# Kernel optimization log

Hardware: AMD Instinct MI355X
Metric: run time of the kernel (lower is better)

Reference implementation:

```python
import jax, jax.numpy as jnp
import numpy as np

N, C_S, C_Z, H, D = 512, 384, 128, 16, 24  # c_hidden per head
EPS = 1e-5

def _ln(x, g, b):
    m = jnp.mean(x, axis=-1, keepdims=True)
    v = jnp.mean(jnp.square(x - m), axis=-1, keepdims=True)
    return (x - m) * jax.lax.rsqrt(v + EPS) * g + b

def setup_inputs() -> dict:
    key = jax.random.key(0)
    ks = jax.random.split(key, 12)
    s = lambda fan: 1.0 / np.sqrt(fan)
    return {
        "a": jax.random.normal(ks[0], (1, N, C_S), jnp.float32),
        "z": jax.random.normal(ks[1], (1, N, N, C_Z), jnp.float32),
        "g_a": jnp.ones((C_S,), jnp.float32),
        "b_a": jnp.zeros((C_S,), jnp.float32),
        "g_z": jnp.ones((C_Z,), jnp.float32),
        "b_z": jnp.zeros((C_Z,), jnp.float32),
        "Wz": jax.random.normal(ks[2], (C_Z, H), jnp.float32) * s(C_Z),
        "bz": jnp.zeros((H,), jnp.float32),
        "Wq": jax.random.normal(ks[3], (C_S, H * D), jnp.float32) * s(C_S),
        "Wk": jax.random.normal(ks[4], (C_S, H * D), jnp.float32) * s(C_S),
        "Wv": jax.random.normal(ks[5], (C_S, H * D), jnp.float32) * s(C_S),
        "Wg": jax.random.normal(ks[6], (C_S, H * D), jnp.float32) * s(C_S),
        "bg": jnp.zeros((H * D,), jnp.float32),
        "Wo": jax.random.normal(ks[7], (H * D, C_S), jnp.float32) * s(H * D),
        "bo": jnp.zeros((C_S,), jnp.float32),
    }

def reference(a, z, g_a, b_a, g_z, b_z, Wz, bz, Wq, Wk, Wv, Wg, bg, Wo, bo):
    B = a.shape[0]
    a_n = _ln(a, g_a, b_a)                       # [B,N,C_S]
    z_n = _ln(z, g_z, b_z)                       # [B,N,N,C_Z]
    # linear_z then permute(0,3,1,2): [B,N,N,H] -> [B,H,N,N]
    pair_bias = jnp.einsum('bijc,ch->bhij', z_n, Wz) + bz[None, :, None, None]
    q = (a_n @ Wq).reshape(B, N, H, D) * (1.0 / np.sqrt(D))
    k = (a_n @ Wk).reshape(B, N, H, D)
    v = (a_n @ Wv).reshape(B, N, H, D)
    scores = jnp.einsum('bqhd,bkhd->bhqk', q, k) + pair_bias
    p = jax.nn.softmax(scores, axis=-1)
    o = jnp.einsum('bhqk,bkhd->bqhd', p, v)      # [B,N,H,D]
    g = jax.nn.sigmoid(a_n @ Wg + bg).reshape(B, N, H, D)
    o = (o * g).reshape(B, N, H * D)
    return o @ Wo + bo                            # [B,N,C_S]
```

## Files before the change

kernel.cpp:

```cpp
#include <hip/hip_runtime.h>
#include <math.h>

#define N 512
#define CS 384
#define CZ 128
#define NH 16
#define DH 24
#define HD 384
#define NN (N*N)
#define EPS 1e-5f

#define OFF_AN   0
#define OFF_QT   196608
#define OFF_KT   393216
#define OFF_VT   589824
#define OFF_GT   786432
#define OFF_OG   983040
#define OFF_WZ2  1179648
#define OFF_SH   1181696
#define OFF_BH   1181712
#define OFF_BIAS 1181728

__global__ void prep_kernel(const float* __restrict__ g_z, const float* __restrict__ lnb_z,
                            const float* __restrict__ Wz, const float* __restrict__ bz,
                            float* __restrict__ wz2, float* __restrict__ sh, float* __restrict__ bh) {
    int t = threadIdx.x;
    for (int i = t; i < NH * CZ; i += 256) {
        int h = i >> 7, c = i & (CZ - 1);
        wz2[h * CZ + c] = g_z[c] * Wz[c * NH + h];
    }
    __shared__ float ls[NH][17], lb[NH][17];
    int h = t >> 4, seg = t & 15;
    float s = 0.f, b = 0.f;
    #pragma unroll
    for (int i = 0; i < 8; ++i) {
        int c = seg * 8 + i;
        float w = Wz[c * NH + h];
        s += g_z[c] * w;
        b += lnb_z[c] * w;
    }
    ls[h][seg] = s; lb[h][seg] = b;
    __syncthreads();
    if (t < NH) {
        float ss = 0.f, bb = 0.f;
        #pragma unroll
        for (int i = 0; i < 16; ++i) { ss += ls[t][i]; bb += lb[t][i]; }
        sh[t] = ss;
        bh[t] = bb + bz[t];
    }
}

__global__ void ln_a_kernel(const float* __restrict__ a, const float* __restrict__ g_a,
                            const float* __restrict__ b_a, float* __restrict__ an_out) {
    int r = blockIdx.x, t = threadIdx.x;
    const float* row = a + r * CS;
    float x0 = row[t], x1 = row[t + 128], x2 = row[t + 256];
    float s1 = x0 + x1 + x2;
    float s2 = x0 * x0 + x1 * x1 + x2 * x2;
    #pragma unroll
    for (int m = 1; m < 64; m <<= 1) {
        s1 += __shfl_xor(s1, m, 64);
        s2 += __shfl_xor(s2, m, 64);
    }
    __shared__ float ls1[2], ls2[2];
    if ((t & 63) == 0) { ls1[t >> 6] = s1; ls2[t >> 6] = s2; }
    __syncthreads();
    s1 = ls1[0] + ls1[1];
    s2 = ls2[0] + ls2[1];
    float mu = s1 * (1.f / CS);
    float var = s2 * (1.f / CS) - mu * mu;
    float rs = rsqrtf(var + EPS);
    float* an = an_out + r * CS;
    an[t]       = (x0 - mu) * rs * g_a[t]       + b_a[t];
    an[t + 128] = (x1 - mu) * rs * g_a[t + 128] + b_a[t + 128];
    an[t + 256] = (x2 - mu) * rs * g_a[t + 256] + b_a[t + 256];
}

__global__ void __launch_bounds__(256) qkvg_kernel(const float* __restrict__ Wq, const float* __restrict__ Wk,
                                                   const float* __restrict__ Wv, const float* __restrict__ Wg,
                                                   const float* __restrict__ bg, const float* __restrict__ an,
                                                   float* __restrict__ qt, float* __restrict__ ktd,
                                                   float* __restrict__ vtd, float* __restrict__ gt) {
    const int lane = threadIdx.x & 63;
    const int w = __builtin_amdgcn_readfirstlane(threadIdx.x >> 6);
    const int strip = blockIdx.x * 4 + w;
    const int n0 = strip * 8;
    const int sel = n0 / HD;
    const int col = n0 % HD;
    const float* Wm = (sel == 0) ? Wq : (sel == 1) ? Wk : (sel == 2) ? Wv : Wg;
    const int m = blockIdx.y * 64 + lane;
    const float* arow = an + m * CS;
    float acc[8];
    #pragma unroll
    for (int j = 0; j < 8; ++j) acc[j] = 0.f;
    for (int kb = 0; kb < CS; kb += 32) {
        float4 av[8];
        #pragma unroll
        for (int i = 0; i < 8; ++i) av[i] = ((const float4*)(arow + kb))[i];
        #pragma unroll
        for (int i = 0; i < 8; ++i) {
            const float* wr = Wm + (kb + i * 4) * HD + col;
            #pragma unroll
            for (int j = 0; j < 8; ++j) {
                acc[j] += av[i].x * wr[j];
                acc[j] += av[i].y * wr[HD + j];
                acc[j] += av[i].z * wr[2 * HD + j];
                acc[j] += av[i].w * wr[3 * HD + j];
            }
        }
    }
    if (sel == 0) {
        #pragma unroll
        for (int j = 0; j < 8; ++j) {
            int c = col + j;
            qt[((c / DH) * N + m) * DH + (c % DH)] = acc[j] * 0.20412414523193153f;
        }
    } else if (sel == 3) {
        #pragma unroll
        for (int j = 0; j < 8; ++j) {
            int c = col + j;
            gt[((c / DH) * N + m) * DH + (c % DH)] = 1.f / (1.f + __expf(-(acc[j] + bg[col + j])));
        }
    } else {
        float* dst = (sel == 1) ? ktd : vtd;
        #pragma unroll
        for (int j = 0; j < 8; ++j) {
            int c = col + j;
            dst[((c / DH) * DH + (c % DH)) * N + m] = acc[j];
        }
    }
}

__global__ void __launch_bounds__(256) pairbias_kernel(const float* __restrict__ z,
                                                       const float* __restrict__ wz2,
                                                       const float* __restrict__ sh,
                                                       const float* __restrict__ bh,
                                                       float* __restrict__ bias) {
    const int row = blockIdx.x * 256 + threadIdx.x;
    const float* zr = z + (size_t)row * CZ;
    float dots[NH];
    #pragma unroll
    for (int h = 0; h < NH; ++h) dots[h] = 0.f;
    float s1 = 0.f, s2 = 0.f;
    #pragma unroll
    for (int cb = 0; cb < CZ; cb += 32) {
        float4 zv[8];
        #pragma unroll
        for (int i = 0; i < 8; ++i) zv[i] = ((const float4*)(zr + cb))[i];
        #pragma unroll
        for (int i = 0; i < 8; ++i) {
            s1 += zv[i].x + zv[i].y + zv[i].z + zv[i].w;
            s2 += zv[i].x * zv[i].x + zv[i].y * zv[i].y + zv[i].z * zv[i].z + zv[i].w * zv[i].w;
        }
        #pragma unroll
        for (int h = 0; h < NH; ++h) {
            const float* wrow = wz2 + h * CZ + cb;
            float d = dots[h];
            #pragma unroll
            for (int i = 0; i < 8; ++i) {
                d += zv[i].x * wrow[i * 4 + 0];
                d += zv[i].y * wrow[i * 4 + 1];
                d += zv[i].z * wrow[i * 4 + 2];
                d += zv[i].w * wrow[i * 4 + 3];
            }
            dots[h] = d;
        }
    }
    float mu = s1 * (1.f / CZ);
    float var = s2 * (1.f / CZ) - mu * mu;
    float r = rsqrtf(var + EPS);
    #pragma unroll
    for (int h = 0; h < NH; ++h)
        bias[h * NN + row] = r * (dots[h] - mu * sh[h]) + bh[h];
}

__global__ void __launch_bounds__(256) attn_kernel(const float* __restrict__ qt, const float* __restrict__ ktd,
                                                   const float* __restrict__ vtd, const float* __restrict__ gt,
                                                   const float* __restrict__ bias, float* __restrict__ og) {
    const int lane = threadIdx.x & 63;
    const int w = __builtin_amdgcn_readfirstlane(threadIdx.x >> 6);
    const int qhalf = lane >> 5;
    const int kl = lane & 31;
    const int h = blockIdx.y;
    const int q = blockIdx.x * 8 + w * 2 + qhalf;
    const float* qT  = qt  + h * N * DH;
    const float* kTd = ktd + h * DH * N;
    const float* vTd = vtd + h * DH * N;

    float qv[DH];
    #pragma unroll
    for (int d6 = 0; d6 < 6; ++d6) {
        float4 t4 = ((const float4*)(qT + q * DH))[d6];
        qv[d6 * 4 + 0] = t4.x; qv[d6 * 4 + 1] = t4.y; qv[d6 * 4 + 2] = t4.z; qv[d6 * 4 + 3] = t4.w;
    }
    float sc[16];
    #pragma unroll
    for (int t = 0; t < 4; ++t) {
        const int kbase = t * 128 + kl * 4;
        float4 b4 = *(const float4*)(bias + h * NN + q * N + kbase);
        float s0 = b4.x, s1 = b4.y, s2 = b4.z, s3 = b4.w;
        #pragma unroll
        for (int d = 0; d < DH; ++d) {
            float4 k4 = *(const float4*)(kTd + d * N + kbase);
            float qd = qv[d];
            s0 += qd * k4.x; s1 += qd * k4.y; s2 += qd * k4.z; s3 += qd * k4.w;
        }
        sc[t * 4 + 0] = s0; sc[t * 4 + 1] = s1; sc[t * 4 + 2] = s2; sc[t * 4 + 3] = s3;
    }
    float mx = sc[0];
    #pragma unroll
    for (int t = 1; t < 16; ++t) mx = fmaxf(mx, sc[t]);
    #pragma unroll
    for (int m = 1; m < 32; m <<= 1) mx = fmaxf(mx, __shfl_xor(mx, m, 64));
    float sum = 0.f;
    #pragma unroll
    for (int t = 0; t < 16; ++t) { sc[t] = __expf(sc[t] - mx); sum += sc[t]; }
    #pragma unroll
    for (int m = 1; m < 32; m <<= 1) sum += __shfl_xor(sum, m, 64);
    float inv = 1.f / sum;
    #pragma unroll
    for (int t = 0; t < 16; ++t) sc[t] *= inv;
    float acc[DH];
    #pragma unroll
    for (int d = 0; d < DH; ++d) acc[d] = 0.f;
    #pragma unroll
    for (int t = 0; t < 4; ++t) {
        const int kbase = t * 128 + kl * 4;
        float p0 = sc[t * 4 + 0], p1 = sc[t * 4 + 1], p2 = sc[t * 4 + 2], p3 = sc[t * 4 + 3];
        #pragma unroll
        for (int d = 0; d < DH; ++d) {
            float4 v4 = *(const float4*)(vTd + d * N + kbase);
            acc[d] += p0 * v4.x + p1 * v4.y + p2 * v4.z + p3 * v4.w;
        }
    }
    #pragma unroll
    for (int m = 1; m < 32; m <<= 1) {
        #pragma unroll
        for (int d = 0; d < DH; ++d) acc[d] += __shfl_xor(acc[d], m, 64);
    }
    float o = 0.f;
    #pragma unroll
    for (int d = 0; d < DH; ++d) o = (kl == d) ? acc[d] : o;
    if (kl < DH) {
        float g = gt[h * N * DH + q * DH + kl];
        og[q * HD + h * DH + kl] = o * g;
    }
}

__global__ void __launch_bounds__(256) out_gemm_kernel(const float* __restrict__ Wo, const float* __restrict__ bo,
                                                       const float* __restrict__ og, float* __restrict__ out) {
    const int lane = threadIdx.x & 63;
    const int w = __builtin_amdgcn_readfirstlane(threadIdx.x >> 6);
    const int strip = blockIdx.x * 4 + w;
    const int c0 = strip * 4;
    const int m = blockIdx.y * 64 + lane;
    const float* orow = og + m * HD;
    float acc[4];
    #pragma unroll
    for (int j = 0; j < 4; ++j) acc[j] = 0.f;
    for (int kb = 0; kb < HD; kb += 32) {
        float4 av[8];
        #pragma unroll
        for (int i = 0; i < 8; ++i) av[i] = ((const float4*)(orow + kb))[i];
        #pragma unroll
        for (int i = 0; i < 8; ++i) {
            const float* wr = Wo + (kb + i * 4) * CS + c0;
            #pragma unroll
            for (int j = 0; j < 4; ++j) {
                acc[j] += av[i].x * wr[j];
                acc[j] += av[i].y * wr[CS + j];
                acc[j] += av[i].z * wr[2 * CS + j];
                acc[j] += av[i].w * wr[3 * CS + j];
            }
        }
    }
    #pragma unroll
    for (int j = 0; j < 4; ++j) out[m * CS + c0 + j] = acc[j] + bo[c0 + j];
}

extern "C" void kernel_launch(void* const* d_in, const int* in_sizes, int n_in,
                              void* d_out, int out_size, void* d_ws, size_t ws_size,
                              hipStream_t stream) {
    const float* a    = (const float*)d_in[0];
    const float* z    = (const float*)d_in[1];
    const float* g_a  = (const float*)d_in[2];
    const float* b_a  = (const float*)d_in[3];
    const float* g_z  = (const float*)d_in[4];
    const float* b_z  = (const float*)d_in[5];
    const float* Wz   = (const float*)d_in[6];
    const float* bz   = (const float*)d_in[7];
    const float* Wq   = (const float*)d_in[8];
    const float* Wk   = (const float*)d_in[9];
    const float* Wv   = (const float*)d_in[10];
    const float* Wg   = (const float*)d_in[11];
    const float* bg   = (const float*)d_in[12];
    const float* Wo   = (const float*)d_in[13];
    const float* bo   = (const float*)d_in[14];
    float* ws  = (float*)d_ws;
    float* out = (float*)d_out;

    float* an   = ws + OFF_AN;
    float* qt   = ws + OFF_QT;
    float* ktd  = ws + OFF_KT;
    float* vtd  = ws + OFF_VT;
    float* gt   = ws + OFF_GT;
    float* ogp  = ws + OFF_OG;
    float* wz2  = ws + OFF_WZ2;
    float* shp  = ws + OFF_SH;
    float* bhp  = ws + OFF_BH;
    float* bias = ws + OFF_BIAS;

    hipLaunchKernelGGL(prep_kernel,     dim3(1),      dim3(256), 0, stream, g_z, b_z, Wz, bz, wz2, shp, bhp);
    hipLaunchKernelGGL(ln_a_kernel,     dim3(512),    dim3(128), 0, stream, a, g_a, b_a, an);
    hipLaunchKernelGGL(qkvg_kernel,     dim3(48, 8),  dim3(256), 0, stream, Wq, Wk, Wv, Wg, bg, an, qt, ktd, vtd, gt);
    hipLaunchKernelGGL(pairbias_kernel, dim3(1024),   dim3(256), 0, stream, z, wz2, shp, bhp, bias);
    hipLaunchKernelGGL(attn_kernel,     dim3(64, 16), dim3(256), 0, stream, qt, ktd, vtd, gt, bias, ogp);
    hipLaunchKernelGGL(out_gemm_kernel, dim3(24, 8),  dim3(256), 0, stream, Wo, bo, ogp, out);
}
```

Before: 366.5 us.

## Fuse pair-bias computation into attention kernel via shared-memory bias tile

Merges the pair-bias kernel into the attention kernel. Each block now handles one query row and computes that row's 512x16 bias from z directly into shared memory, then runs all 16 heads with 16 lanes per head. This removes the write and reread of the 16 MB bias tensor in global memory. The cost is a large shared-memory footprint (about 34 KB per block), which limits occupancy. The attention phase also uses fewer lanes per head, so each thread does more serial work, and only 512 blocks are launched.

```diff
diff --git a/kernel.cpp b/kernel.cpp
--- a/kernel.cpp
+++ b/kernel.cpp
@@ -19,7 +19,6 @@
 #define OFF_WZ2  1179648
 #define OFF_SH   1181696
 #define OFF_BH   1181712
-#define OFF_BIAS 1181728
 
 __global__ void prep_kernel(const float* __restrict__ g_z, const float* __restrict__ lnb_z,
                             const float* __restrict__ Wz, const float* __restrict__ bz,
@@ -126,125 +125,136 @@
         #pragma unroll
         for (int j = 0; j < 8; ++j) {
             int c = col + j;
-            dst[((c / DH) * DH + (c % DH)) * N + m] = acc[j];
-        }
-    }
-}
-
-__global__ void __launch_bounds__(256) pairbias_kernel(const float* __restrict__ z,
+            dst[c * N + m] = acc[j];
+        }
+    }
+}
+
+__global__ void __launch_bounds__(256) pairattn_kernel(const float* __restrict__ z,
                                                        const float* __restrict__ wz2,
                                                        const float* __restrict__ sh,
                                                        const float* __restrict__ bh,
-                                                       float* __restrict__ bias) {
-    const int row = blockIdx.x * 256 + threadIdx.x;
-    const float* zr = z + (size_t)row * CZ;
-    float dots[NH];
-    #pragma unroll
-    for (int h = 0; h < NH; ++h) dots[h] = 0.f;
-    float s1 = 0.f, s2 = 0.f;
-    #pragma unroll
-    for (int cb = 0; cb < CZ; cb += 32) {
-        float4 zv[8];
-        #pragma unroll
-        for (int i = 0; i < 8; ++i) zv[i] = ((const float4*)(zr + cb))[i];
-        #pragma unroll
-        for (int i = 0; i < 8; ++i) {
-            s1 += zv[i].x + zv[i].y + zv[i].z + zv[i].w;
-            s2 += zv[i].x * zv[i].x + zv[i].y * zv[i].y + zv[i].z * zv[i].z + zv[i].w * zv[i].w;
-        }
-        #pragma unroll
-        for (int h = 0; h < NH; ++h) {
-            const float* wrow = wz2 + h * CZ + cb;
-            float d = dots[h];
+                                                       const float* __restrict__ qt,
+                                                       const float* __restrict__ ktd,
+                                                       const float* __restrict__ vtd,
+                                                       const float* __restrict__ gt,
+                                                       float* __restrict__ og) {
+    __shared__ float bias_lds[N * 17];
+    const int q = blockIdx.x;
+    const int t = threadIdx.x;
+
+    #pragma unroll
+    for (int rr = 0; rr < 2; ++rr) {
+        const int k = t + rr * 256;
+        const float* zr = z + ((size_t)q * N + k) * CZ;
+        float dots[NH];
+        #pragma unroll
+        for (int h = 0; h < NH; ++h) dots[h] = 0.f;
+        float s1 = 0.f, s2 = 0.f;
+        #pragma unroll
+        for (int cb = 0; cb < CZ; cb += 32) {
+            float4 zv[8];
+            #pragma unroll
+            for (int i = 0; i < 8; ++i) zv[i] = ((const float4*)(zr + cb))[i];
             #pragma unroll
             for (int i = 0; i < 8; ++i) {
-                d += zv[i].x * wrow[i * 4 + 0];
-                d += zv[i].y * wrow[i * 4 + 1];
-                d += zv[i].z * wrow[i * 4 + 2];
-                d += zv[i].w * wrow[i * 4 + 3];
+                s1 += zv[i].x + zv[i].y + zv[i].z + zv[i].w;
+                s2 += zv[i].x * zv[i].x + zv[i].y * zv[i].y + zv[i].z * zv[i].z + zv[i].w * zv[i].w;
             }
-            dots[h] = d;
-        }
-    }
-    float mu = s1 * (1.f / CZ);
-    float var = s2 * (1.f / CZ) - mu * mu;
-    float r = rsqrtf(var + EPS);
-    #pragma unroll
-    for (int h = 0; h < NH; ++h)
-        bias[h * NN + row] = r * (dots[h] - mu * sh[h]) + bh[h];
-}
-
-__global__ void __launch_bounds__(256) attn_kernel(const float* __restrict__ qt, const float* __restrict__ ktd,
-                                                   const float* __restrict__ vtd, const float* __restrict__ gt,
-                                                   const float* __restrict__ bias, float* __restrict__ og) {
-    const int lane = threadIdx.x & 63;
-    const int w = __builtin_amdgcn_readfirstlane(threadIdx.x >> 6);
-    const int qhalf = lane >> 5;
-    const int kl = lane & 31;
-    const int h = blockIdx.y;
-    const int q = blockIdx.x * 8 + w * 2 + qhalf;
-    const float* qT  = qt  + h * N * DH;
+            #pragma unroll
+            for (int h = 0; h < NH; ++h) {
+                const float* wrow = wz2 + h * CZ + cb;
+                float d = dots[h];
+                #pragma unroll
+                for (int i = 0; i < 8; ++i) {
+                    d += zv[i].x * wrow[i * 4 + 0];
+                    d += zv[i].y * wrow[i * 4 + 1];
+                    d += zv[i].z * wrow[i * 4 + 2];
+                    d += zv[i].w * wrow[i * 4 + 3];
+                }
+                dots[h] = d;
+            }
+        }
+        float mu = s1 * (1.f / CZ);
+        float var = s2 * (1.f / CZ) - mu * mu;
+        float r = rsqrtf(var + EPS);
+        #pragma unroll
+        for (int h = 0; h < NH; ++h)
+            bias_lds[k * 17 + h] = r * (dots[h] - mu * sh[h]) + bh[h];
+    }
+    __syncthreads();
+
+    const int h = t >> 4;
+    const int l = t & 15;
     const float* kTd = ktd + h * DH * N;
     const float* vTd = vtd + h * DH * N;
 
     float qv[DH];
     #pragma unroll
     for (int d6 = 0; d6 < 6; ++d6) {
-        float4 t4 = ((const float4*)(qT + q * DH))[d6];
+        float4 t4 = ((const float4*)(qt + (h * N + q) * DH))[d6];
         qv[d6 * 4 + 0] = t4.x; qv[d6 * 4 + 1] = t4.y; qv[d6 * 4 + 2] = t4.z; qv[d6 * 4 + 3] = t4.w;
     }
-    float sc[16];
-    #pragma unroll
-    for (int t = 0; t < 4; ++t) {
-        const int kbase = t * 128 + kl * 4;
-        float4 b4 = *(const float4*)(bias + h * NN + q * N + kbase);
-        float s0 = b4.x, s1 = b4.y, s2 = b4.z, s3 = b4.w;
-        #pragma unroll
-        for (int d = 0; d < DH; ++d) {
-            float4 k4 = *(const float4*)(kTd + d * N + kbase);
-            float qd = qv[d];
-            s0 += qd * k4.x; s1 += qd * k4.y; s2 += qd * k4.z; s3 += qd * k4.w;
-        }
-        sc[t * 4 + 0] = s0; sc[t * 4 + 1] = s1; sc[t * 4 + 2] = s2; sc[t * 4 + 3] = s3;
+    float sc[32];
+    #pragma unroll
+    for (int j = 0; j < 8; ++j) {
+        #pragma unroll
+        for (int i = 0; i < 4; ++i)
+            sc[j * 4 + i] = bias_lds[(j * 64 + l * 4 + i) * 17 + h];
+    }
+    #pragma unroll
+    for (int d = 0; d < DH; ++d) {
+        const float* kd = kTd + d * N + l * 4;
+        float qd = qv[d];
+        #pragma unroll
+        for (int j = 0; j < 8; ++j) {
+            float4 k4 = *(const float4*)(kd + j * 64);
+            sc[j * 4 + 0] += qd * k4.x;
+            sc[j * 4 + 1] += qd * k4.y;
+            sc[j * 4 + 2] += qd * k4.z;
+            sc[j * 4 + 3] += qd * k4.w;
+        }
     }
     float mx = sc[0];
     #pragma unroll
-    for (int t = 1; t < 16; ++t) mx = fmaxf(mx, sc[t]);
-    #pragma unroll
-    for (int m = 1; m < 32; m <<= 1) mx = fmaxf(mx, __shfl_xor(mx, m, 64));
+    for (int u = 1; u < 32; ++u) mx = fmaxf(mx, sc[u]);
+    #pragma unroll
+    for (int m = 1; m < 16; m <<= 1) mx = fmaxf(mx, __shfl_xor(mx, m, 64));
     float sum = 0.f;
     #pragma unroll
-    for (int t = 0; t < 16; ++t) { sc[t] = __expf(sc[t] - mx); sum += sc[t]; }
-    #pragma unroll
-    for (int m = 1; m < 32; m <<= 1) sum += __shfl_xor(sum, m, 64);
+    for (int u = 0; u < 32; ++u) { sc[u] = __expf(sc[u] - mx); sum += sc[u]; }
+    #pragma unroll
+    for (int m = 1; m < 16; m <<= 1) sum += __shfl_xor(sum, m, 64);
     float inv = 1.f / sum;
-    #pragma unroll
-    for (int t = 0; t < 16; ++t) sc[t] *= inv;
     float acc[DH];
     #pragma unroll
     for (int d = 0; d < DH; ++d) acc[d] = 0.f;
     #pragma unroll
-    for (int t = 0; t < 4; ++t) {
-        const int kbase = t * 128 + kl * 4;
-        float p0 = sc[t * 4 + 0], p1 = sc[t * 4 + 1], p2 = sc[t * 4 + 2], p3 = sc[t * 4 + 3];
-        #pragma unroll
-        for (int d = 0; d < DH; ++d) {
-            float4 v4 = *(const float4*)(vTd + d * N + kbase);
-            acc[d] += p0 * v4.x + p1 * v4.y + p2 * v4.z + p3 * v4.w;
-        }
-    }
-    #pragma unroll
-    for (int m = 1; m < 32; m <<= 1) {
+    for (int d = 0; d < DH; ++d) {
+        const float* vd = vTd + d * N + l * 4;
+        float a = 0.f;
+        #pragma unroll
+        for (int j = 0; j < 8; ++j) {
+            float4 v4 = *(const float4*)(vd + j * 64);
+            a += sc[j * 4 + 0] * v4.x + sc[j * 4 + 1] * v4.y
+               + sc[j * 4 + 2] * v4.z + sc[j * 4 + 3] * v4.w;
+        }
+        acc[d] = a;
+    }
+    #pragma unroll
+    for (int m = 1; m < 16; m <<= 1) {
         #pragma unroll
         for (int d = 0; d < DH; ++d) acc[d] += __shfl_xor(acc[d], m, 64);
     }
-    float o = 0.f;
-    #pragma unroll
-    for (int d = 0; d < DH; ++d) o = (kl == d) ? acc[d] : o;
-    if (kl < DH) {
-        float g = gt[h * N * DH + q * DH + kl];
-        og[q * HD + h * DH + kl] = o * g;
-    }
+    float o1 = 0.f, o2 = 0.f;
+    #pragma unroll
+    for (int d = 0; d < 16; ++d) o1 = (l == d) ? acc[d] : o1;
+    #pragma unroll
+    for (int d = 16; d < 24; ++d) o2 = (l == (d - 16)) ? acc[d] : o2;
+    const float* gq = gt + (h * N + q) * DH;
+    og[q * HD + h * DH + l] = o1 * inv * gq[l];
+    if (l < 8)
+        og[q * HD + h * DH + 16 + l] = o2 * inv * gq[16 + l];
 }
 
 __global__ void __launch_bounds__(256) out_gemm_kernel(const float* __restrict__ Wo, const float* __restrict__ bo,
@@ -308,12 +318,10 @@
     float* wz2  = ws + OFF_WZ2;
     float* shp  = ws + OFF_SH;
     float* bhp  = ws + OFF_BH;
-    float* bias = ws + OFF_BIAS;
 
     hipLaunchKernelGGL(prep_kernel,     dim3(1),      dim3(256), 0, stream, g_z, b_z, Wz, bz, wz2, shp, bhp);
     hipLaunchKernelGGL(ln_a_kernel,     dim3(512),    dim3(128), 0, stream, a, g_a, b_a, an);
     hipLaunchKernelGGL(qkvg_kernel,     dim3(48, 8),  dim3(256), 0, stream, Wq, Wk, Wv, Wg, bg, an, qt, ktd, vtd, gt);
-    hipLaunchKernelGGL(pairbias_kernel, dim3(1024),   dim3(256), 0, stream, z, wz2, shp, bhp, bias);
-    hipLaunchKernelGGL(attn_kernel,     dim3(64, 16), dim3(256), 0, stream, qt, ktd, vtd, gt, bias, ogp);
+    hipLaunchKernelGGL(pairattn_kernel, dim3(512),    dim3(256), 0, stream, z, wz2, shp, bhp, qt, ktd, vtd, gt, ogp);
     hipLaunchKernelGGL(out_gemm_kernel, dim3(24, 8),  dim3(256), 0, stream, Wo, bo, ogp, out);
 }
```

Result: slower. 1.041 ms (+184.1%).
